# Performance work log

Measured on AMD Instinct MI355X. Metric: run time of the kernel, lower is better.

The kernel has to match this reference:

```python
import jax, jax.numpy as jnp
import numpy as np

H = 32  # hidden_size from LSTMConfig

def setup_inputs() -> dict:
    key = jax.random.key(0)
    ks = jax.random.split(key, 7)
    B, T, F = 131072, 22, 12
    s = 1.0 / np.sqrt(H)
    return {
        "x": jax.random.normal(ks[0], (B, T, F), dtype=jnp.float32),
        "W_ih": jax.random.uniform(ks[1], (4 * H, F), minval=-s, maxval=s, dtype=jnp.float32),
        "W_hh": jax.random.uniform(ks[2], (4 * H, H), minval=-s, maxval=s, dtype=jnp.float32),
        "b_ih": jax.random.uniform(ks[3], (4 * H,), minval=-s, maxval=s, dtype=jnp.float32),
        "b_hh": jax.random.uniform(ks[4], (4 * H,), minval=-s, maxval=s, dtype=jnp.float32),
        "W_head": jax.random.uniform(ks[5], (1, H), minval=-s, maxval=s, dtype=jnp.float32),
        "b_head": jax.random.uniform(ks[6], (1,), minval=-s, maxval=s, dtype=jnp.float32),
    }

def _lstm_last_hidden(x, W_ih, W_hh, b_ih, b_hh):
    B, T, F = x.shape
    # precompute input contribution for all timesteps: [T, B, 4H]
    gx = jnp.einsum('btf,gf->tbg', x, W_ih) + (b_ih + b_hh)

    def step(carry, gx_t):
        h, c = carry
        g = gx_t + h @ W_hh.T                      # [B, 4H]
        i, f, gg, o = jnp.split(g, 4, axis=-1)     # PyTorch gate order i,f,g,o
        i = jax.nn.sigmoid(i)
        f = jax.nn.sigmoid(f)
        gg = jnp.tanh(gg)
        o = jax.nn.sigmoid(o)
        c = f * c + i * gg
        h = o * jnp.tanh(c)
        return (h, c), None

    h0 = jnp.zeros((B, H), dtype=x.dtype)
    (h, _), _ = jax.lax.scan(step, (h0, h0), gx)
    return h  # [B, H] last timestep hidden

def reference(x, W_ih, W_hh, b_ih, b_hh, W_head, b_head):
    h = _lstm_last_hidden(x, W_ih, W_hh, b_ih, b_hh)
    # Dropout p=0.0 is identity; Linear(H,1) + Softplus, then squeeze(-1)
    y = h @ W_head.T + b_head                      # [B, 1]
    return jax.nn.softplus(y)[:, 0]                # [B]
```

## Files before the change

### kernel.cpp

```cpp
#include <hip/hip_runtime.h>
#include <math.h>

#define T_STEPS 22
#define F_IN    12
#define HID     32

typedef __attribute__((ext_vector_type(8))) short  bf16x8;
typedef __attribute__((ext_vector_type(16))) float f32x16;

union FragU { unsigned int u[4]; bf16x8 v; };

#define LOG2E    1.442695041f
#define TWOLOG2E 2.885390082f

static __device__ __forceinline__ unsigned short f2bf(float x) {
    unsigned int u = __builtin_bit_cast(unsigned int, x);
    return (unsigned short)((u + 0x7fffu + ((u >> 16) & 1u)) >> 16);
}

static __device__ __forceinline__ unsigned cvt_pk_bf16(float lo, float hi) {
    unsigned r;
    asm("v_cvt_pk_bf16_f32 %0, %1, %2" : "=v"(r) : "v"(lo), "v"(hi));
    return r;
}

static __device__ __forceinline__ float bf2f(short s) {
    return __builtin_bit_cast(float, ((unsigned)(unsigned short)s) << 16);
}

__global__ void prep_kernel(const float* __restrict__ Wih, const float* __restrict__ Whh,
                            const float* __restrict__ bih, const float* __restrict__ bhh,
                            const float* __restrict__ Whead, float* __restrict__ ws) {
    const int tid = threadIdx.x;
    unsigned short* wx = (unsigned short*)ws;
    unsigned short* wh = (unsigned short*)(ws + 1024);
    float* whd = ws + 3072;

    {
        int m = tid >> 6, lane = tid & 63;
        int g = 32 * m + (lane & 31);
        float scale = (m == 2) ? TWOLOG2E : -LOG2E;
        int kbase = 8 * (lane >> 5);
        for (int j = 0; j < 8; ++j) {
            int k = kbase + j;
            float v = 0.0f;
            if (k < F_IN)       v = Wih[g * F_IN + k];
            else if (k == F_IN) v = bih[g] + bhh[g];
            wx[tid * 8 + j] = f2bf(scale * v);
        }
    }
    for (int e = tid; e < 4 * 2 * 64; e += 256) {
        int m = e >> 7, kt = (e >> 6) & 1, lane = e & 63;
        int g = 32 * m + (lane & 31);
        float scale = (m == 2) ? TWOLOG2E : -LOG2E;
        int kbase = 16 * kt + 8 * (lane >> 5);
        for (int j = 0; j < 8; ++j)
            wh[e * 8 + j] = f2bf(scale * Whh[g * HID + kbase + j]);
    }
    if (tid < 32) {
        int h2 = tid >> 4, j = tid & 15;
        int k = (j < 8) ? (8 * h2 + j) : (16 + 8 * h2 + (j - 8));
        whd[tid] = Whead[k];
    }
}

__global__ void __launch_bounds__(256, 2)
lstm_kernel(const float* __restrict__ x, const float* __restrict__ ws,
            const float* __restrict__ bheadp, float* __restrict__ out, int B) {
    const int tid  = threadIdx.x;
    const int lane = tid & 63;
    const int wave = tid >> 6;
    const int col  = lane & 31;
    const int hi   = lane >> 5;
    int b = blockIdx.x * 128 + wave * 32 + col;
    const bool valid = (b < B);
    if (b >= B) b = B - 1;

    __shared__ float wlds[3072];
#pragma unroll
    for (int i = 0; i < 3; ++i)
        ((float4*)wlds)[tid + i * 256] = ((const float4*)ws)[tid + i * 256];
    __syncthreads();

    const bf16x8* wx_l = (const bf16x8*)wlds;
    const bf16x8* wh_l = ((const bf16x8*)wlds) + 256;

    const float* xb1 = x + (size_t)b * (T_STEPS * F_IN) + (hi ? 8 : 0);
    const float* xb2 = x + (size_t)b * (T_STEPS * F_IN) + (hi ? 8 : 4);

    float c[16];
#pragma unroll
    for (int q = 0; q < 16; ++q) c[q] = 0.0f;
    bf16x8 hf0, hf1;
#pragma unroll
    for (int j = 0; j < 8; ++j) { hf0[j] = 0; hf1[j] = 0; }

#pragma unroll 1
    for (int t = 0; t < T_STEPS; ++t) {
        asm volatile("" ::: "memory");

        float4 va = *(const float4*)(xb1 + t * F_IN);
        float4 vb = *(const float4*)(xb2 + t * F_IN);
        FragU xf;
        xf.u[0] = cvt_pk_bf16(va.x, va.y);
        xf.u[1] = cvt_pk_bf16(va.z, va.w);
        unsigned w2 = cvt_pk_bf16(vb.x, vb.y);
        unsigned w3 = cvt_pk_bf16(vb.z, vb.w);
        xf.u[2] = hi ? 0x00003f80u : w2;
        xf.u[3] = hi ? 0u : w3;

        f32x16 a0, a1, a2, a3;
#pragma unroll
        for (int q = 0; q < 16; ++q) { a0[q] = 0.f; a1[q] = 0.f; a2[q] = 0.f; a3[q] = 0.f; }

        a0 = __builtin_amdgcn_mfma_f32_32x32x16_bf16(wx_l[0 * 64 + lane], xf.v, a0, 0, 0, 0);
        a1 = __builtin_amdgcn_mfma_f32_32x32x16_bf16(wx_l[1 * 64 + lane], xf.v, a1, 0, 0, 0);
        a2 = __builtin_amdgcn_mfma_f32_32x32x16_bf16(wx_l[2 * 64 + lane], xf.v, a2, 0, 0, 0);
        a3 = __builtin_amdgcn_mfma_f32_32x32x16_bf16(wx_l[3 * 64 + lane], xf.v, a3, 0, 0, 0);
        a0 = __builtin_amdgcn_mfma_f32_32x32x16_bf16(wh_l[(0 * 2 + 0) * 64 + lane], hf0, a0, 0, 0, 0);
        a1 = __builtin_amdgcn_mfma_f32_32x32x16_bf16(wh_l[(1 * 2 + 0) * 64 + lane], hf0, a1, 0, 0, 0);
        a2 = __builtin_amdgcn_mfma_f32_32x32x16_bf16(wh_l[(2 * 2 + 0) * 64 + lane], hf0, a2, 0, 0, 0);
        a3 = __builtin_amdgcn_mfma_f32_32x32x16_bf16(wh_l[(3 * 2 + 0) * 64 + lane], hf0, a3, 0, 0, 0);
        a0 = __builtin_amdgcn_mfma_f32_32x32x16_bf16(wh_l[(0 * 2 + 1) * 64 + lane], hf1, a0, 0, 0, 0);
        a1 = __builtin_amdgcn_mfma_f32_32x32x16_bf16(wh_l[(1 * 2 + 1) * 64 + lane], hf1, a1, 0, 0, 0);
        a2 = __builtin_amdgcn_mfma_f32_32x32x16_bf16(wh_l[(2 * 2 + 1) * 64 + lane], hf1, a2, 0, 0, 0);
        a3 = __builtin_amdgcn_mfma_f32_32x32x16_bf16(wh_l[(3 * 2 + 1) * 64 + lane], hf1, a3, 0, 0, 0);
        __builtin_amdgcn_sched_group_barrier(0x100, 4, 0);
        __builtin_amdgcn_sched_group_barrier(0x008, 4, 0);
        __builtin_amdgcn_sched_group_barrier(0x100, 4, 0);
        __builtin_amdgcn_sched_group_barrier(0x008, 4, 0);
        __builtin_amdgcn_sched_group_barrier(0x100, 4, 0);
        __builtin_amdgcn_sched_group_barrier(0x008, 4, 0);

        unsigned P[8];
#pragma unroll
        for (int p = 0; p < 8; ++p) {
            const int q0 = 2 * p, q1 = 2 * p + 1;
            float ri0 = __builtin_amdgcn_rcpf(1.0f + __builtin_amdgcn_exp2f(a0[q0]));
            float rf0 = __builtin_amdgcn_rcpf(1.0f + __builtin_amdgcn_exp2f(a1[q0]));
            float rg0 = __builtin_amdgcn_rcpf(1.0f + __builtin_amdgcn_exp2f(a2[q0]));
            float ro0 = __builtin_amdgcn_rcpf(1.0f + __builtin_amdgcn_exp2f(a3[q0]));
            float gs0 = fmaf(-2.0f * TWOLOG2E, rg0, TWOLOG2E);
            c[q0] = fmaf(rf0, c[q0], ri0 * gs0);
            float tc0 = fmaf(-2.0f, __builtin_amdgcn_rcpf(1.0f + __builtin_amdgcn_exp2f(c[q0])), 1.0f);
            float hv0 = ro0 * tc0;

            float ri1 = __builtin_amdgcn_rcpf(1.0f + __builtin_amdgcn_exp2f(a0[q1]));
            float rf1 = __builtin_amdgcn_rcpf(1.0f + __builtin_amdgcn_exp2f(a1[q1]));
            float rg1 = __builtin_amdgcn_rcpf(1.0f + __builtin_amdgcn_exp2f(a2[q1]));
            float ro1 = __builtin_amdgcn_rcpf(1.0f + __builtin_amdgcn_exp2f(a3[q1]));
            float gs1 = fmaf(-2.0f * TWOLOG2E, rg1, TWOLOG2E);
            c[q1] = fmaf(rf1, c[q1], ri1 * gs1);
            float tc1 = fmaf(-2.0f, __builtin_amdgcn_rcpf(1.0f + __builtin_amdgcn_exp2f(c[q1])), 1.0f);
            float hv1 = ro1 * tc1;

            P[p] = cvt_pk_bf16(hv0, hv1);
        }

        asm("v_permlane32_swap_b32 %0, %1" : "+v"(P[0]), "+v"(P[2]));
        asm("v_permlane32_swap_b32 %0, %1" : "+v"(P[1]), "+v"(P[3]));
        asm("v_permlane32_swap_b32 %0, %1" : "+v"(P[4]), "+v"(P[6]));
        asm("v_permlane32_swap_b32 %0, %1" : "+v"(P[5]), "+v"(P[7]));
        FragU h0; h0.u[0] = P[0]; h0.u[1] = P[1]; h0.u[2] = P[2]; h0.u[3] = P[3];
        FragU h1; h1.u[0] = P[4]; h1.u[1] = P[5]; h1.u[2] = P[6]; h1.u[3] = P[7];
        hf0 = h0.v;
        hf1 = h1.v;
    }

    const float* whd = ws + 3072 + hi * 16;
    float y = 0.0f;
#pragma unroll
    for (int j = 0; j < 8; ++j) {
        y = fmaf(bf2f(hf0[j]), whd[j], y);
        y = fmaf(bf2f(hf1[j]), whd[8 + j], y);
    }
    y += __shfl_xor(y, 32, 64);
    y += bheadp[0];
    float sp = fmaxf(y, 0.0f) + log1pf(expf(-fabsf(y)));
    if (valid && hi == 0) out[b] = sp;
}

extern "C" void kernel_launch(void* const* d_in, const int* in_sizes, int n_in,
                              void* d_out, int out_size, void* d_ws, size_t ws_size,
                              hipStream_t stream) {
    const float* x     = (const float*)d_in[0];
    const float* Wih   = (const float*)d_in[1];
    const float* Whh   = (const float*)d_in[2];
    const float* bih   = (const float*)d_in[3];
    const float* bhh   = (const float*)d_in[4];
    const float* Whead = (const float*)d_in[5];
    const float* bhead = (const float*)d_in[6];
    float* out = (float*)d_out;
    float* ws  = (float*)d_ws;

    const int B = in_sizes[0] / (T_STEPS * F_IN);
    const int blocks = (B + 127) / 128;

    hipLaunchKernelGGL(prep_kernel, dim3(1), dim3(256), 0, stream,
                       Wih, Whh, bih, bhh, Whead, ws);
    hipLaunchKernelGGL(lstm_kernel, dim3(blocks), dim3(256), 0, stream,
                       x, ws, bhead, out, B);
}
```

Before: 97.43 us.

## Merge LSTM gate reciprocals algebraically, pack math into float2, prefetch next x

Rewrites the gate nonlinearities so the i, f and g sigmoids share one reciprocal and the o-gate and tanh(c) share another, cutting reciprocal count per element from five to two. The elementwise math is written on float2 vectors so the compiler can emit packed FP32 ops. The next timestep's x is loaded one iteration ahead, MFMA accumulators start from a hoisted zero vector, and the manual sched_group_barrier hints are removed. The merged form multiplies several (1+exp) factors together, which risks overflow to inf for large pre-activations and may change numerics slightly.

```diff
diff --git a/kernel.cpp b/kernel.cpp
--- a/kernel.cpp
+++ b/kernel.cpp
@@ -7,6 +7,7 @@
 
 typedef __attribute__((ext_vector_type(8))) short  bf16x8;
 typedef __attribute__((ext_vector_type(16))) float f32x16;
+typedef __attribute__((ext_vector_type(2)))  float f32x2;
 
 union FragU { unsigned int u[4]; bf16x8 v; };
 
@@ -24,8 +25,8 @@
     return r;
 }
 
-static __device__ __forceinline__ float bf2f(short s) {
-    return __builtin_bit_cast(float, ((unsigned)(unsigned short)s) << 16);
+static __device__ __forceinline__ float bf2f(short s_) {
+    return __builtin_bit_cast(float, ((unsigned)(unsigned short)s_) << 16);
 }
 
 __global__ void prep_kernel(const float* __restrict__ Wih, const float* __restrict__ Whh,
@@ -82,25 +83,36 @@
         ((float4*)wlds)[tid + i * 256] = ((const float4*)ws)[tid + i * 256];
     __syncthreads();
 
-    const bf16x8* wx_l = (const bf16x8*)wlds;
-    const bf16x8* wh_l = ((const bf16x8*)wlds) + 256;
-
     const float* xb1 = x + (size_t)b * (T_STEPS * F_IN) + (hi ? 8 : 0);
     const float* xb2 = x + (size_t)b * (T_STEPS * F_IN) + (hi ? 8 : 4);
 
-    float c[16];
-#pragma unroll
-    for (int q = 0; q < 16; ++q) c[q] = 0.0f;
+    f32x2 c2[8];
+#pragma unroll
+    for (int p = 0; p < 8; ++p) c2[p] = (f32x2){0.f, 0.f};
     bf16x8 hf0, hf1;
 #pragma unroll
     for (int j = 0; j < 8; ++j) { hf0[j] = 0; hf1[j] = 0; }
+
+    f32x16 zc;
+#pragma unroll
+    for (int q = 0; q < 16; ++q) zc[q] = 0.0f;
+
+    const f32x2 one2 = {1.0f, 1.0f};
+
+    float4 va = *(const float4*)(xb1);
+    float4 vb = *(const float4*)(xb2);
 
 #pragma unroll 1
     for (int t = 0; t < T_STEPS; ++t) {
-        asm volatile("" ::: "memory");
-
-        float4 va = *(const float4*)(xb1 + t * F_IN);
-        float4 vb = *(const float4*)(xb2 + t * F_IN);
+        int zr = 0;
+        asm("" : "+v"(zr));
+        const bf16x8* wx_l = ((const bf16x8*)wlds) + zr;
+        const bf16x8* wh_l = ((const bf16x8*)wlds) + 256 + zr;
+
+        const int tn = (t + 1 < T_STEPS) ? t + 1 : t;
+        float4 na = *(const float4*)(xb1 + tn * F_IN);
+        float4 nb = *(const float4*)(xb2 + tn * F_IN);
+
         FragU xf;
         xf.u[0] = cvt_pk_bf16(va.x, va.y);
         xf.u[1] = cvt_pk_bf16(va.z, va.w);
@@ -110,13 +122,10 @@
         xf.u[3] = hi ? 0u : w3;
 
         f32x16 a0, a1, a2, a3;
-#pragma unroll
-        for (int q = 0; q < 16; ++q) { a0[q] = 0.f; a1[q] = 0.f; a2[q] = 0.f; a3[q] = 0.f; }
-
-        a0 = __builtin_amdgcn_mfma_f32_32x32x16_bf16(wx_l[0 * 64 + lane], xf.v, a0, 0, 0, 0);
-        a1 = __builtin_amdgcn_mfma_f32_32x32x16_bf16(wx_l[1 * 64 + lane], xf.v, a1, 0, 0, 0);
-        a2 = __builtin_amdgcn_mfma_f32_32x32x16_bf16(wx_l[2 * 64 + lane], xf.v, a2, 0, 0, 0);
-        a3 = __builtin_amdgcn_mfma_f32_32x32x16_bf16(wx_l[3 * 64 + lane], xf.v, a3, 0, 0, 0);
+        a0 = __builtin_amdgcn_mfma_f32_32x32x16_bf16(wx_l[0 * 64 + lane], xf.v, zc, 0, 0, 0);
+        a1 = __builtin_amdgcn_mfma_f32_32x32x16_bf16(wx_l[1 * 64 + lane], xf.v, zc, 0, 0, 0);
+        a2 = __builtin_amdgcn_mfma_f32_32x32x16_bf16(wx_l[2 * 64 + lane], xf.v, zc, 0, 0, 0);
+        a3 = __builtin_amdgcn_mfma_f32_32x32x16_bf16(wx_l[3 * 64 + lane], xf.v, zc, 0, 0, 0);
         a0 = __builtin_amdgcn_mfma_f32_32x32x16_bf16(wh_l[(0 * 2 + 0) * 64 + lane], hf0, a0, 0, 0, 0);
         a1 = __builtin_amdgcn_mfma_f32_32x32x16_bf16(wh_l[(1 * 2 + 0) * 64 + lane], hf0, a1, 0, 0, 0);
         a2 = __builtin_amdgcn_mfma_f32_32x32x16_bf16(wh_l[(2 * 2 + 0) * 64 + lane], hf0, a2, 0, 0, 0);
@@ -125,36 +134,27 @@
         a1 = __builtin_amdgcn_mfma_f32_32x32x16_bf16(wh_l[(1 * 2 + 1) * 64 + lane], hf1, a1, 0, 0, 0);
         a2 = __builtin_amdgcn_mfma_f32_32x32x16_bf16(wh_l[(2 * 2 + 1) * 64 + lane], hf1, a2, 0, 0, 0);
         a3 = __builtin_amdgcn_mfma_f32_32x32x16_bf16(wh_l[(3 * 2 + 1) * 64 + lane], hf1, a3, 0, 0, 0);
-        __builtin_amdgcn_sched_group_barrier(0x100, 4, 0);
-        __builtin_amdgcn_sched_group_barrier(0x008, 4, 0);
-        __builtin_amdgcn_sched_group_barrier(0x100, 4, 0);
-        __builtin_amdgcn_sched_group_barrier(0x008, 4, 0);
-        __builtin_amdgcn_sched_group_barrier(0x100, 4, 0);
-        __builtin_amdgcn_sched_group_barrier(0x008, 4, 0);
 
         unsigned P[8];
 #pragma unroll
         for (int p = 0; p < 8; ++p) {
             const int q0 = 2 * p, q1 = 2 * p + 1;
-            float ri0 = __builtin_amdgcn_rcpf(1.0f + __builtin_amdgcn_exp2f(a0[q0]));
-            float rf0 = __builtin_amdgcn_rcpf(1.0f + __builtin_amdgcn_exp2f(a1[q0]));
-            float rg0 = __builtin_amdgcn_rcpf(1.0f + __builtin_amdgcn_exp2f(a2[q0]));
-            float ro0 = __builtin_amdgcn_rcpf(1.0f + __builtin_amdgcn_exp2f(a3[q0]));
-            float gs0 = fmaf(-2.0f * TWOLOG2E, rg0, TWOLOG2E);
-            c[q0] = fmaf(rf0, c[q0], ri0 * gs0);
-            float tc0 = fmaf(-2.0f, __builtin_amdgcn_rcpf(1.0f + __builtin_amdgcn_exp2f(c[q0])), 1.0f);
-            float hv0 = ro0 * tc0;
-
-            float ri1 = __builtin_amdgcn_rcpf(1.0f + __builtin_amdgcn_exp2f(a0[q1]));
-            float rf1 = __builtin_amdgcn_rcpf(1.0f + __builtin_amdgcn_exp2f(a1[q1]));
-            float rg1 = __builtin_amdgcn_rcpf(1.0f + __builtin_amdgcn_exp2f(a2[q1]));
-            float ro1 = __builtin_amdgcn_rcpf(1.0f + __builtin_amdgcn_exp2f(a3[q1]));
-            float gs1 = fmaf(-2.0f * TWOLOG2E, rg1, TWOLOG2E);
-            c[q1] = fmaf(rf1, c[q1], ri1 * gs1);
-            float tc1 = fmaf(-2.0f, __builtin_amdgcn_rcpf(1.0f + __builtin_amdgcn_exp2f(c[q1])), 1.0f);
-            float hv1 = ro1 * tc1;
-
-            P[p] = cvt_pk_bf16(hv0, hv1);
+            f32x2 ei = {__builtin_amdgcn_exp2f(a0[q0]), __builtin_amdgcn_exp2f(a0[q1])};
+            f32x2 ef = {__builtin_amdgcn_exp2f(a1[q0]), __builtin_amdgcn_exp2f(a1[q1])};
+            f32x2 eg = {__builtin_amdgcn_exp2f(a2[q0]), __builtin_amdgcn_exp2f(a2[q1])};
+            f32x2 eo = {__builtin_amdgcn_exp2f(a3[q0]), __builtin_amdgcn_exp2f(a3[q1])};
+            f32x2 A  = (one2 + ei) * (one2 + eg);
+            f32x2 F  = one2 + ef;
+            f32x2 FA = F * A;
+            f32x2 r1 = {__builtin_amdgcn_rcpf(FA.x), __builtin_amdgcn_rcpf(FA.y)};
+            f32x2 t2 = eg * (f32x2){TWOLOG2E, TWOLOG2E} - (f32x2){TWOLOG2E, TWOLOG2E};
+            f32x2 num = t2 * F + c2[p] * A;
+            c2[p] = num * r1;
+            f32x2 ec = {__builtin_amdgcn_exp2f(c2[p].x), __builtin_amdgcn_exp2f(c2[p].y)};
+            f32x2 r2in = (one2 + eo) * (one2 + ec);
+            f32x2 r2 = {__builtin_amdgcn_rcpf(r2in.x), __builtin_amdgcn_rcpf(r2in.y)};
+            f32x2 hv = (ec - one2) * r2;
+            P[p] = cvt_pk_bf16(hv.x, hv.y);
         }
 
         asm("v_permlane32_swap_b32 %0, %1" : "+v"(P[0]), "+v"(P[2]));
@@ -165,13 +165,15 @@
         FragU h1; h1.u[0] = P[4]; h1.u[1] = P[5]; h1.u[2] = P[6]; h1.u[3] = P[7];
         hf0 = h0.v;
         hf1 = h1.v;
+
+        va = na; vb = nb;
     }
 
     const float* whd = ws + 3072 + hi * 16;
     float y = 0.0f;
 #pragma unroll
     for (int j = 0; j < 8; ++j) {
-        y = fmaf(bf2f(hf0[j]), whd[j], y);
+        y = fmaf(bf2f(hf0[j]), whd[j],     y);
         y = fmaf(bf2f(hf1[j]), whd[8 + j], y);
     }
     y += __shfl_xor(y, 32, 64);
```

After: 88.14 us. 9.5% less time.
